# Kernel tuning notes

Measured on AMD Instinct MI355X. Metric: run time of the kernel, lower is better.

The kernel has to match this reference:

```python
import jax, jax.numpy as jnp
import numpy as np

ALPHA = 0.1   # synaptic current decay
BETA = 0.96   # membrane decay
V_THR = 2.0   # firing threshold


def setup_inputs() -> dict:
    key = jax.random.key(0)
    T, B, N = 512, 32, 4096
    x = jax.random.normal(key, (T, B, N), dtype=jnp.float32)
    return {"x": x}


def reference(x):
    """snntorch Synaptic neuron scan, reset_mechanism='zero'.

    Per step (snntorch semantics):
      reset   = heaviside(mem_prev - thr)           (spike from previous mem)
      syn'    = alpha*syn + x_t
      mem'    = beta*mem + syn'
      zero reset: syn' -= reset*syn'; mem' -= reset*mem'
      spk     = heaviside(mem' - thr)
    """
    dt = x.dtype

    def step(carry, xt):
        syn, mem = carry
        reset = (mem > V_THR).astype(dt)
        syn_n = ALPHA * syn + xt
        mem_n = BETA * mem + syn_n
        syn_n = syn_n * (1.0 - reset)
        mem_n = mem_n * (1.0 - reset)
        spk = (mem_n > V_THR).astype(dt)
        return (syn_n, mem_n), (spk, syn_n, mem_n)

    init = (jnp.zeros_like(x[0]), jnp.zeros_like(x[0]))
    _, (spk, syn, mem) = jax.lax.scan(step, init, x)
    return spk, syn, mem
```

## Files before the change

kernel.cpp:

```cpp
#include <hip/hip_runtime.h>


#define T_STEPS 512
#define BN      131072
#define NT4     (BN / 4)

__global__ __launch_bounds__(64) void snn_synaptic_kernel(
    const float4* __restrict__ x, float* __restrict__ out) {
  const int i = blockIdx.x * 64 + threadIdx.x;

  float4* __restrict__ spk_o = (float4*)out;
  float4* __restrict__ syn_o = (float4*)(out + (long long)T_STEPS * BN);
  float4* __restrict__ mem_o = (float4*)(out + 2LL * T_STEPS * BN);

  float4 syn = make_float4(0.f, 0.f, 0.f, 0.f);
  float4 mem = make_float4(0.f, 0.f, 0.f, 0.f);

  float4 xc = x[i];

  #pragma unroll 4
  for (int t = 0; t < T_STEPS; ++t) {
    const int tn = (t + 1 < T_STEPS) ? (t + 1) : t;
    float4 xn = x[(long long)tn * NT4 + i];

    float4 spk;
    #define STEP(c)                                                  \
      {                                                              \
        const float keep = (mem.c > 2.0f) ? 0.0f : 1.0f;             \
        syn.c = __fadd_rn(__fmul_rn(0.1f, syn.c), xc.c);             \
        mem.c = __fadd_rn(__fmul_rn(0.96f, mem.c), syn.c);           \
        syn.c *= keep;                                               \
        mem.c *= keep;                                               \
        spk.c = (mem.c > 2.0f) ? 1.0f : 0.0f;                        \
      }
    STEP(x) STEP(y) STEP(z) STEP(w)
    #undef STEP

    const long long o = (long long)t * NT4 + i;
    spk_o[o] = spk;
    syn_o[o] = syn;
    mem_o[o] = mem;

    xc = xn;
  }
}

extern "C" void kernel_launch(void* const* d_in, const int* in_sizes, int n_in,
                              void* d_out, int out_size, void* d_ws, size_t ws_size,
                              hipStream_t stream) {
  const float4* x = (const float4*)d_in[0];
  float* out = (float*)d_out;
  snn_synaptic_kernel<<<dim3(NT4 / 64), dim3(64), 0, stream>>>(x, out);
}
```

Measured before the change: 967.8 us.

## Use one neuron per thread with four-step prefetch and nontemporal stores

Switches from four neurons per thread (float4) to one neuron per thread, which raises the thread count fourfold and uses 256-thread blocks. Input is prefetched four time steps ahead, so more loads are in flight to hide the latency of the sequential scan. Outputs are written with nontemporal stores to avoid polluting the cache with streamed data. The trade-off is scalar instead of vector memory accesses, though wavefront-level accesses stay coalesced.

```diff
diff --git a/kernel.cpp b/kernel.cpp
--- a/kernel.cpp
+++ b/kernel.cpp
@@ -3,52 +3,53 @@
 
 #define T_STEPS 512
 #define BN      131072
-#define NT4     (BN / 4)
 
-__global__ __launch_bounds__(64) void snn_synaptic_kernel(
-    const float4* __restrict__ x, float* __restrict__ out) {
-  const int i = blockIdx.x * 64 + threadIdx.x;
+__global__ __launch_bounds__(256) void snn_synaptic_kernel(
+    const float* __restrict__ x, float* __restrict__ out) {
+  const int i = blockIdx.x * 256 + threadIdx.x;
 
-  float4* __restrict__ spk_o = (float4*)out;
-  float4* __restrict__ syn_o = (float4*)(out + (long long)T_STEPS * BN);
-  float4* __restrict__ mem_o = (float4*)(out + 2LL * T_STEPS * BN);
+  float* __restrict__ spk_o = out;
+  float* __restrict__ syn_o = out + (long long)T_STEPS * BN;
+  float* __restrict__ mem_o = out + 2LL * T_STEPS * BN;
 
-  float4 syn = make_float4(0.f, 0.f, 0.f, 0.f);
-  float4 mem = make_float4(0.f, 0.f, 0.f, 0.f);
+  float syn = 0.f, mem = 0.f;
 
-  float4 xc = x[i];
+  float x0 = x[i];
+  float x1 = x[1 * BN + i];
+  float x2 = x[2 * BN + i];
+  float x3 = x[3 * BN + i];
 
-  #pragma unroll 4
-  for (int t = 0; t < T_STEPS; ++t) {
-    const int tn = (t + 1 < T_STEPS) ? (t + 1) : t;
-    float4 xn = x[(long long)tn * NT4 + i];
+  for (int t = 0; t < T_STEPS; t += 4) {
+    const int pb = ((t + 4 < T_STEPS) ? (t + 4) : t) * BN + i;
+    const float n0 = x[pb];
+    const float n1 = x[pb + BN];
+    const float n2 = x[pb + 2 * BN];
+    const float n3 = x[pb + 3 * BN];
 
-    float4 spk;
-    #define STEP(c)                                                  \
-      {                                                              \
-        const float keep = (mem.c > 2.0f) ? 0.0f : 1.0f;             \
-        syn.c = __fadd_rn(__fmul_rn(0.1f, syn.c), xc.c);             \
-        mem.c = __fadd_rn(__fmul_rn(0.96f, mem.c), syn.c);           \
-        syn.c *= keep;                                               \
-        mem.c *= keep;                                               \
-        spk.c = (mem.c > 2.0f) ? 1.0f : 0.0f;                        \
+    #define STEP(tt, XV)                                           \
+      {                                                            \
+        const float keep = (mem > 2.0f) ? 0.0f : 1.0f;             \
+        syn = __fadd_rn(__fmul_rn(0.1f, syn), XV);                 \
+        mem = __fadd_rn(__fmul_rn(0.96f, mem), syn);               \
+        syn *= keep;                                               \
+        mem *= keep;                                               \
+        const float spk = (mem > 2.0f) ? 1.0f : 0.0f;              \
+        const int o = (tt) * BN + i;                               \
+        __builtin_nontemporal_store(spk, spk_o + o);               \
+        __builtin_nontemporal_store(syn, syn_o + o);               \
+        __builtin_nontemporal_store(mem, mem_o + o);               \
       }
-    STEP(x) STEP(y) STEP(z) STEP(w)
+    STEP(t + 0, x0) STEP(t + 1, x1) STEP(t + 2, x2) STEP(t + 3, x3)
     #undef STEP
 
-    const long long o = (long long)t * NT4 + i;
-    spk_o[o] = spk;
-    syn_o[o] = syn;
-    mem_o[o] = mem;
-
-    xc = xn;
+    x0 = n0; x1 = n1; x2 = n2; x3 = n3;
   }
 }
 
 extern "C" void kernel_launch(void* const* d_in, const int* in_sizes, int n_in,
                               void* d_out, int out_size, void* d_ws, size_t ws_size,
                               hipStream_t stream) {
-  const float4* x = (const float4*)d_in[0];
+  const float* x = (const float*)d_in[0];
   float* out = (float*)d_out;
-  snn_synaptic_kernel<<<dim3(NT4 / 64), dim3(64), 0, stream>>>(x, out);
+  snn_synaptic_kernel<<<dim3(BN / 256), dim3(256), 0, stream>>>(x, out);
 }
```

Measured after the change: 954.9 us. About the same (-1.3%).
